# Kernel optimization log

Hardware: AMD Instinct MI355X
Metric: run time of the kernel (lower is better)

Reference implementation:

```python
import jax, jax.numpy as jnp
import numpy as np

BETA = 0.95
THR = 1.0
NUM_STEPS = 100
ALPHA = 2.0  # snntorch atan surrogate default

@jax.custom_vjp
def atan_spike(x):
    return (x > 0).astype(x.dtype)

def _as_fwd(x):
    return (x > 0).astype(x.dtype), x

def _as_bwd(x, g):
    return (g * (ALPHA / 2) / (1 + (jnp.pi / 2 * ALPHA * x) ** 2),)

atan_spike.defvjp(_as_fwd, _as_bwd)


def setup_inputs() -> dict:
    key = jax.random.key(0)
    ks = jax.random.split(key, 9)
    B = 16384
    SH, NH, CO, OUT = 1024, 1024, 256, 64
    s = 0.05
    return {
        "x": jax.random.normal(ks[0], (B, 105), jnp.float32),
        "snn_w1": jax.random.normal(ks[1], (SH, 5), jnp.float32) * s,
        "snn_b1": jnp.zeros((SH,), jnp.float32),
        "snn_w2": jax.random.normal(ks[2], (OUT, SH), jnp.float32) * s,
        "snn_b2": jnp.zeros((OUT,), jnp.float32),
        "nn_w1": jax.random.normal(ks[3], (NH, 5), jnp.float32) * s,
        "nn_b1": jnp.zeros((NH,), jnp.float32),
        "nn_w2": jax.random.normal(ks[4], (OUT, NH), jnp.float32) * s,
        "nn_b2": jnp.zeros((OUT,), jnp.float32),
        "conv_w": jax.random.normal(ks[5], (32, 1, 3), jnp.float32) * s,
        "conv_b": jnp.zeros((32,), jnp.float32),
        "cnn_fc_w": jax.random.normal(ks[6], (CO, 32 * 50), jnp.float32) * s,
        "cnn_fc_b": jnp.zeros((CO,), jnp.float32),
        "comb_w": jax.random.normal(ks[7], (OUT, 2 * OUT + CO), jnp.float32) * s,
        "comb_b": jnp.zeros((OUT,), jnp.float32),
    }


def _forward(x, snn_w1, snn_b1, snn_w2, snn_b2, nn_w1, nn_b1, nn_w2, nn_b2,
             conv_w, conv_b, cnn_fc_w, cnn_fc_b, comb_w, comb_b):
    feats = x[:, :5]                 # [B,5]
    wave = x[:, 5:][:, None, :]      # [B,1,100]
    B = x.shape[0]

    # ---- SNN branch (LIF, beta leak, subtract reset, threshold 1.0) ----
    cur1 = feats @ snn_w1.T + snn_b1  # input current is constant across steps

    def step(carry, _):
        mem1, spk1, mem2, spk2 = carry
        # reset term uses detached spike (snntorch mem_reset detaches)
        mem1 = BETA * mem1 + cur1 - jax.lax.stop_gradient(spk1) * THR
        spk1 = atan_spike(mem1 - THR)
        cur2 = spk1 @ snn_w2.T + snn_b2
        mem2 = BETA * mem2 + cur2 - jax.lax.stop_gradient(spk2) * THR
        spk2 = atan_spike(mem2 - THR)
        return (mem1, spk1, mem2, spk2), spk2

    z1 = jnp.zeros_like(cur1)
    z2 = jnp.zeros((B, snn_w2.shape[0]), cur1.dtype)
    _, spk_rec = jax.lax.scan(step, (z1, z1, z2, z2), None, length=NUM_STEPS)
    snn_out = spk_rec.mean(axis=0)   # [B,OUT]

    # ---- MLP branch ----
    nn_out = jax.nn.relu(feats @ nn_w1.T + nn_b1) @ nn_w2.T + nn_b2

    # ---- CNN branch ----
    c = jax.lax.conv_general_dilated(wave, conv_w, (1,), [(1, 1)],
                                     dimension_numbers=("NCW", "OIW", "NCW"))
    c = jax.nn.relu(c + conv_b[None, :, None])   # [B,32,100]
    c = c.reshape(B, 32, 50, 2).max(axis=-1)      # MaxPool1d(k=2,s=2)
    cnn_out = c.reshape(B, -1) @ cnn_fc_w.T + cnn_fc_b

    combined = jnp.concatenate([snn_out, nn_out, cnn_out], axis=1)
    return combined @ comb_w.T + comb_b


def reference(x, snn_w1, snn_b1, snn_w2, snn_b2, nn_w1, nn_b1, nn_w2, nn_b2,
              conv_w, conv_b, cnn_fc_w, cnn_fc_b, comb_w, comb_b):
    return _forward(x, snn_w1, snn_b1, snn_w2, snn_b2, nn_w1, nn_b1, nn_w2,
                    nn_b2, conv_w, conv_b, cnn_fc_w, cnn_fc_b, comb_w, comb_b)
```

## Files before the change

kernel.cpp:

```cpp
#include <hip/hip_runtime.h>

typedef __bf16 bf16x8_t __attribute__((ext_vector_type(8)));
typedef float f32x4_t __attribute__((ext_vector_type(4)));

#define NSTEPS 100
#define COMBF 51200u

static __device__ __forceinline__ unsigned short f2bfu(float v) {
  union { __bf16 h; unsigned short u; } c; c.h = (__bf16)v; return c.u;
}
static __device__ __forceinline__ unsigned int pack2bf(float a, float b) {
  return (unsigned)f2bfu(a) | ((unsigned)f2bfu(b) << 16);
}
union BF8U { unsigned int u[4]; bf16x8_t v; };

static __device__ __forceinline__ bf16x8_t bfrag_f32(const float* __restrict__ p, float s) {
  BF8U r;
#pragma unroll
  for (int i = 0; i < 4; ++i) r.u[i] = pack2bf(p[2*i]*s, p[2*i+1]*s);
  return r.v;
}

static __device__ __forceinline__ void comb_store(unsigned char* ldsp, int k, int row, float v) {
  *(unsigned short*)(ldsp + COMBF +
      (unsigned)((k >> 5)*1024 + (((k >> 3) & 3)*16 + row)*16 + (k & 7)*2)) = f2bfu(v);
}

__global__ __launch_bounds__(512, 2)
void hybrid_v3(const float* __restrict__ x,
               const float* __restrict__ snn_w1, const float* __restrict__ snn_b1,
               const float* __restrict__ snn_w2, const float* __restrict__ snn_b2,
               const float* __restrict__ nn_w1,  const float* __restrict__ nn_b1,
               const float* __restrict__ nn_w2,  const float* __restrict__ nn_b2,
               const float* __restrict__ conv_w, const float* __restrict__ conv_b,
               const float* __restrict__ fc_w,   const float* __restrict__ fc_b,
               const float* __restrict__ comb_w, const float* __restrict__ comb_b,
               const unsigned short* __restrict__ fcwb, int use_bf,
               float* __restrict__ out)
{
  __shared__ __align__(16) unsigned char lds[65536];
  const int tid  = threadIdx.x;
  const int w    = tid >> 6;
  const int l    = tid & 63;
  const int q    = l >> 4;
  const int m    = l & 15;
  const int row0 = blockIdx.x * 16;

  const int hi  = w >> 2;
  const int ntr = w & 3;
  const int rn  = ntr*16 + m;
  const int rA  = hi*4 + q;
  const int rB  = rA + 8;

  const float* xr = x + (row0 + m)*105;
  const float f0 = xr[0], f1 = xr[1], f2 = xr[2], f3 = xr[3], f4 = xr[4];
  const float b2l = snn_b2[rn];

  bf16x8_t bfr[4][4];
#pragma unroll
  for (int ci = 0; ci < 4; ++ci)
#pragma unroll
    for (int nt = 0; nt < 4; ++nt)
      bfr[ci][nt] = bfrag_f32(snn_w2 + (nt*16 + m)*1024 + (w*4 + ci)*32 + q*8, 1.f);

  float c[32], mem[32];
  {
    const int kb = w*128 + q*8;
#pragma unroll
    for (int ci = 0; ci < 4; ++ci) {
      const float* wp = snn_w1 + (kb + ci*32)*5;
      float wa[40];
#pragma unroll
      for (int u2 = 0; u2 < 10; ++u2) {
        const float4 t4 = *(const float4*)(wp + u2*4);
        wa[u2*4+0] = t4.x; wa[u2*4+1] = t4.y; wa[u2*4+2] = t4.z; wa[u2*4+3] = t4.w;
      }
#pragma unroll
      for (int j = 0; j < 8; ++j) {
        c[ci*8+j] = f0*wa[j*5] + f1*wa[j*5+1] + f2*wa[j*5+2] + f3*wa[j*5+3] + f4*wa[j*5+4]
                  + snn_b1[kb + ci*32 + j];
        mem[ci*8+j] = 0.f;
      }
    }
  }

  BF8U afr[4];
  auto lif_update_pack = [&]() {
#pragma unroll
    for (int i = 0; i < 32; ++i) {
      const float sp = mem[i] > 1.f ? 1.f : 0.f;
      mem[i] = __fsub_rn(__fadd_rn(__fmul_rn(0.95f, mem[i]), c[i]), sp);
    }
#pragma unroll
    for (int ci = 0; ci < 4; ++ci)
#pragma unroll
      for (int jj = 0; jj < 4; ++jj)
        afr[ci].u[jj] = (mem[ci*8 + 2*jj]   > 1.f ? 0x3F80u     : 0u)
                      | (mem[ci*8 + 2*jj+1] > 1.f ? 0x3F800000u : 0u);
  };
  lif_update_pack();

  float m2A = 0.f, s2A = 0.f, cntA = 0.f;
  float m2B = 0.f, s2B = 0.f, cntB = 0.f;

  const unsigned pbase = (unsigned)(ntr*1024 + hi*256 + m*16 + q*4);
  const f32x4_t z4 = {0.f, 0.f, 0.f, 0.f};

#pragma unroll 1
  for (int t = 0; t < NSTEPS; ++t) {
    f32x4_t acc[4] = {z4, z4, z4, z4};
#pragma unroll
    for (int ci = 0; ci < 4; ++ci) {
#pragma unroll
      for (int nt = 0; nt < 4; ++nt)
        acc[nt] = __builtin_amdgcn_mfma_f32_16x16x32_bf16(afr[ci].v, bfr[ci][nt], acc[nt], 0,0,0);
    }
#pragma unroll
    for (int nt = 0; nt < 4; ++nt)
      *(f32x4_t*)(lds + (unsigned)(((w*4 + nt)*64 + l)*16)) = acc[nt];
    __syncthreads();
    float vA[8], vB[8];
#pragma unroll
    for (int s = 0; s < 8; ++s) vA[s] = *(const float*)(lds + pbase + (unsigned)(s*4096));
#pragma unroll
    for (int s = 0; s < 8; ++s) vB[s] = *(const float*)(lds + pbase + 512u + (unsigned)(s*4096));
    if (t < NSTEPS - 1) lif_update_pack();
    {
      float curA = (((vA[0]+vA[1]) + (vA[2]+vA[3])) + ((vA[4]+vA[5]) + (vA[6]+vA[7]))) + b2l;
      float curB = (((vB[0]+vB[1]) + (vB[2]+vB[3])) + ((vB[4]+vB[5]) + (vB[6]+vB[7]))) + b2l;
      m2A = __fsub_rn(__fadd_rn(__fmul_rn(0.95f, m2A), curA), s2A);
      s2A = m2A > 1.f ? 1.f : 0.f;  cntA += s2A;
      m2B = __fsub_rn(__fadd_rn(__fmul_rn(0.95f, m2B), curB), s2B);
      s2B = m2B > 1.f ? 1.f : 0.f;  cntB += s2B;
    }
    __syncthreads();
  }

#pragma unroll
  for (int ci = 0; ci < 4; ++ci)
#pragma unroll
    for (int nt = 0; nt < 4; ++nt)
      bfr[ci][nt] = bfrag_f32(nn_w2 + (nt*16 + m)*1024 + (w*4 + ci)*32 + q*8, 1.f);
  {
    BF8U hfr[4];
    const int kb = w*128 + q*8;
#pragma unroll
    for (int ci = 0; ci < 4; ++ci) {
      const float* wp = nn_w1 + (kb + ci*32)*5;
      float wa[40];
#pragma unroll
      for (int u2 = 0; u2 < 10; ++u2) {
        const float4 t4 = *(const float4*)(wp + u2*4);
        wa[u2*4+0] = t4.x; wa[u2*4+1] = t4.y; wa[u2*4+2] = t4.z; wa[u2*4+3] = t4.w;
      }
      float hv[8];
#pragma unroll
      for (int j = 0; j < 8; ++j) {
        const float h = f0*wa[j*5] + f1*wa[j*5+1] + f2*wa[j*5+2] + f3*wa[j*5+3] + f4*wa[j*5+4]
                      + nn_b1[kb + ci*32 + j];
        hv[j] = fmaxf(h, 0.f);
      }
#pragma unroll
      for (int jj = 0; jj < 4; ++jj) hfr[ci].u[jj] = pack2bf(hv[2*jj], hv[2*jj+1]);
    }
    f32x4_t acc[4] = {z4, z4, z4, z4};
#pragma unroll
    for (int ci = 0; ci < 4; ++ci)
#pragma unroll
      for (int nt = 0; nt < 4; ++nt)
        acc[nt] = __builtin_amdgcn_mfma_f32_16x16x32_bf16(hfr[ci].v, bfr[ci][nt], acc[nt], 0,0,0);
#pragma unroll
    for (int nt = 0; nt < 4; ++nt)
      *(f32x4_t*)(lds + (unsigned)(((w*4 + nt)*64 + l)*16)) = acc[nt];
  }
  __syncthreads();
  {
    float vA[8], vB[8];
#pragma unroll
    for (int s = 0; s < 8; ++s) vA[s] = *(const float*)(lds + pbase + (unsigned)(s*4096));
#pragma unroll
    for (int s = 0; s < 8; ++s) vB[s] = *(const float*)(lds + pbase + 512u + (unsigned)(s*4096));
    const float nA = (((vA[0]+vA[1]) + (vA[2]+vA[3])) + ((vA[4]+vA[5]) + (vA[6]+vA[7]))) + nn_b2[rn];
    const float nB = (((vB[0]+vB[1]) + (vB[2]+vB[3])) + ((vB[4]+vB[5]) + (vB[6]+vB[7]))) + nn_b2[rn];
    comb_store(lds, rn,      rA, cntA * 0.0078125f);
    comb_store(lds, rn,      rB, cntB * 0.0078125f);
    comb_store(lds, 64 + rn, rA, nA);
    comb_store(lds, 64 + rn, rB, nB);
  }
  __syncthreads();

  {
    const int ch = tid >> 4;
    const float cw0 = conv_w[ch*3+0], cw1 = conv_w[ch*3+1], cw2 = conv_w[ch*3+2];
    const float cbb = conv_b[ch];
    const float* xw = xr + 5;
    float xm1 = 0.f, x0v = xw[0];
#pragma unroll 1
    for (int p = 0; p < 50; ++p) {
      const float xp1 = xw[2*p + 1];
      const float xp2 = (p < 49) ? xw[2*p + 2] : 0.f;
      const float av = cw0*xm1 + cw1*x0v + cw2*xp1 + cbb;
      const float bv = cw0*x0v + cw1*xp1 + cw2*xp2 + cbb;
      const float pv = fmaxf(fmaxf(av, 0.f), fmaxf(bv, 0.f));
      const int k = ch*50 + p;
      *(unsigned short*)(lds + (unsigned)((k>>5)*1024 + (((k>>3)&3)*16 + m)*16 + (k&7)*2)) = f2bfu(pv);
      xm1 = xp1; x0v = xp2;
    }
  }
  __syncthreads();

  {
    const int c0 = (w*2 + 0)*16 + m;
    const int c1 = (w*2 + 1)*16 + m;
    f32x4_t e0 = z4, o0 = z4, e1 = z4, o1 = z4;
    if (use_bf) {
#pragma unroll 2
      for (int kc = 0; kc < 50; kc += 2) {
        const bf16x8_t a0 = *(const bf16x8_t*)(lds + (unsigned)((kc*64 + l)*16));
        const bf16x8_t a1 = *(const bf16x8_t*)(lds + (unsigned)(((kc+1)*64 + l)*16));
        e0 = __builtin_amdgcn_mfma_f32_16x16x32_bf16(a0, *(const bf16x8_t*)(fcwb + c0*1600 + kc*32 + q*8), e0, 0,0,0);
        o0 = __builtin_amdgcn_mfma_f32_16x16x32_bf16(a1, *(const bf16x8_t*)(fcwb + c0*1600 + (kc+1)*32 + q*8), o0, 0,0,0);
        e1 = __builtin_amdgcn_mfma_f32_16x16x32_bf16(a0, *(const bf16x8_t*)(fcwb + c1*1600 + kc*32 + q*8), e1, 0,0,0);
        o1 = __builtin_amdgcn_mfma_f32_16x16x32_bf16(a1, *(const bf16x8_t*)(fcwb + c1*1600 + (kc+1)*32 + q*8), o1, 0,0,0);
      }
    } else {
#pragma unroll 2
      for (int kc = 0; kc < 50; kc += 2) {
        const bf16x8_t a0 = *(const bf16x8_t*)(lds + (unsigned)((kc*64 + l)*16));
        const bf16x8_t a1 = *(const bf16x8_t*)(lds + (unsigned)(((kc+1)*64 + l)*16));
        e0 = __builtin_amdgcn_mfma_f32_16x16x32_bf16(a0, bfrag_f32(fc_w + c0*1600 + kc*32 + q*8, 1.f), e0, 0,0,0);
        o0 = __builtin_amdgcn_mfma_f32_16x16x32_bf16(a1, bfrag_f32(fc_w + c0*1600 + (kc+1)*32 + q*8, 1.f), o0, 0,0,0);
        e1 = __builtin_amdgcn_mfma_f32_16x16x32_bf16(a0, bfrag_f32(fc_w + c1*1600 + kc*32 + q*8, 1.f), e1, 0,0,0);
        o1 = __builtin_amdgcn_mfma_f32_16x16x32_bf16(a1, bfrag_f32(fc_w + c1*1600 + (kc+1)*32 + q*8, 1.f), o1, 0,0,0);
      }
    }
    const float fb0 = fc_b[c0], fb1 = fc_b[c1];
#pragma unroll
    for (int r = 0; r < 4; ++r) {
      comb_store(lds, 128 + c0, q*4 + r, (e0[r] + o0[r]) + fb0);
      comb_store(lds, 128 + c1, q*4 + r, (e1[r] + o1[r]) + fb1);
    }
  }
  __syncthreads();

  if (w < 4) {
    const int cn = w*16 + m;
    f32x4_t oe = z4, oo = z4;
#pragma unroll
    for (int kc = 0; kc < 12; kc += 2) {
      const bf16x8_t a0 = *(const bf16x8_t*)(lds + COMBF + (unsigned)((kc*64 + l)*16));
      const bf16x8_t a1 = *(const bf16x8_t*)(lds + COMBF + (unsigned)(((kc+1)*64 + l)*16));
      const float s0 = (kc    < 2) ? 1.28f : 1.f;
      const float s1 = (kc+1 < 2) ? 1.28f : 1.f;
      oe = __builtin_amdgcn_mfma_f32_16x16x32_bf16(a0, bfrag_f32(comb_w + cn*384 + kc*32 + q*8, s0), oe, 0,0,0);
      oo = __builtin_amdgcn_mfma_f32_16x16x32_bf16(a1, bfrag_f32(comb_w + cn*384 + (kc+1)*32 + q*8, s1), oo, 0,0,0);
    }
    const float cb2 = comb_b[cn];
#pragma unroll
    for (int r = 0; r < 4; ++r)
      out[(row0 + q*4 + r)*64 + cn] = (oe[r] + oo[r]) + cb2;
  }
}

__global__ __launch_bounds__(256)
void fcw_to_bf16(const float* __restrict__ src, unsigned short* __restrict__ dst) {
  const int i = (blockIdx.x * 256 + threadIdx.x) * 4;
  const float4 v = *(const float4*)(src + i);
  ushort4 o;
  o.x = f2bfu(v.x); o.y = f2bfu(v.y); o.z = f2bfu(v.z); o.w = f2bfu(v.w);
  *(ushort4*)(dst + i) = o;
}

extern "C" void kernel_launch(void* const* d_in, const int* in_sizes, int n_in,
                              void* d_out, int out_size, void* d_ws, size_t ws_size,
                              hipStream_t stream) {
  const float* x       = (const float*)d_in[0];
  const float* snn_w1  = (const float*)d_in[1];
  const float* snn_b1  = (const float*)d_in[2];
  const float* snn_w2  = (const float*)d_in[3];
  const float* snn_b2  = (const float*)d_in[4];
  const float* nn_w1   = (const float*)d_in[5];
  const float* nn_b1   = (const float*)d_in[6];
  const float* nn_w2   = (const float*)d_in[7];
  const float* nn_b2   = (const float*)d_in[8];
  const float* conv_w  = (const float*)d_in[9];
  const float* conv_b  = (const float*)d_in[10];
  const float* fc_w    = (const float*)d_in[11];
  const float* fc_b    = (const float*)d_in[12];
  const float* comb_w  = (const float*)d_in[13];
  const float* comb_b  = (const float*)d_in[14];
  float* outp = (float*)d_out;

  const int rows = in_sizes[0] / 105;
  const int grid = rows / 16;

  const size_t fcw_elems = (size_t)in_sizes[11];
  const int use_bf = (ws_size >= fcw_elems * 2) ? 1 : 0;
  unsigned short* fcwb = (unsigned short*)d_ws;
  if (use_bf) {
    fcw_to_bf16<<<dim3((unsigned)(fcw_elems / 1024)), dim3(256), 0, stream>>>(fc_w, fcwb);
  }

  hybrid_v3<<<dim3(grid), dim3(512), 0, stream>>>(
      x, snn_w1, snn_b1, snn_w2, snn_b2,
      nn_w1, nn_b1, nn_w2, nn_b2,
      conv_w, conv_b, fc_w, fc_b, comb_w, comb_b,
      fcwb, use_bf, outp);
}
```

Before: 840.7 us.

## Double-buffer SNN partial-sum exchange to halve barriers per timestep

The 100-step LIF loop now ping-pongs between two LDS buffers for the cross-wave partial sums. Each phase reads the previous step's partials while issuing the current step's MFMAs and writes, so one __syncthreads per step is enough instead of two. The second-layer membrane update lags by one step, with a final drain after the loop. This removes a barrier per step and lets LDS reads overlap MFMA work, at the cost of using 64 KB of LDS space for the two buffers plus the combined region and slightly more complex sequencing.

```diff
diff --git a/kernel.cpp b/kernel.cpp
--- a/kernel.cpp
+++ b/kernel.cpp
@@ -4,6 +4,8 @@
 typedef float f32x4_t __attribute__((ext_vector_type(4)));
 
 #define NSTEPS 100
+#define PB0 0u
+#define PB1 32768u
 #define COMBF 51200u
 
 static __device__ __forceinline__ unsigned short f2bfu(float v) {
@@ -27,7 +29,7 @@
 }
 
 __global__ __launch_bounds__(512, 2)
-void hybrid_v3(const float* __restrict__ x,
+void hybrid_v4(const float* __restrict__ x,
                const float* __restrict__ snn_w1, const float* __restrict__ snn_b1,
                const float* __restrict__ snn_w2, const float* __restrict__ snn_b2,
                const float* __restrict__ nn_w1,  const float* __restrict__ nn_b1,
@@ -103,29 +105,29 @@
   float m2A = 0.f, s2A = 0.f, cntA = 0.f;
   float m2B = 0.f, s2B = 0.f, cntB = 0.f;
 
-  const unsigned pbase = (unsigned)(ntr*1024 + hi*256 + m*16 + q*4);
+  const unsigned pbase  = (unsigned)(ntr*1024 + hi*256 + m*16 + q*4);
+  const unsigned wtbase = (unsigned)((w*4*64 + l)*16);
   const f32x4_t z4 = {0.f, 0.f, 0.f, 0.f};
 
-#pragma unroll 1
-  for (int t = 0; t < NSTEPS; ++t) {
+  auto phase = [&](unsigned cur, unsigned prv, bool doRead, bool doLif) {
+    float vA[8], vB[8];
+    if (doRead) {
+#pragma unroll
+      for (int s = 0; s < 8; ++s) vA[s] = *(const float*)(lds + prv + pbase + (unsigned)(s*4096));
+#pragma unroll
+      for (int s = 0; s < 8; ++s) vB[s] = *(const float*)(lds + prv + pbase + 512u + (unsigned)(s*4096));
+    }
     f32x4_t acc[4] = {z4, z4, z4, z4};
 #pragma unroll
-    for (int ci = 0; ci < 4; ++ci) {
+    for (int ci = 0; ci < 4; ++ci)
 #pragma unroll
       for (int nt = 0; nt < 4; ++nt)
         acc[nt] = __builtin_amdgcn_mfma_f32_16x16x32_bf16(afr[ci].v, bfr[ci][nt], acc[nt], 0,0,0);
-    }
 #pragma unroll
     for (int nt = 0; nt < 4; ++nt)
-      *(f32x4_t*)(lds + (unsigned)(((w*4 + nt)*64 + l)*16)) = acc[nt];
-    __syncthreads();
-    float vA[8], vB[8];
-#pragma unroll
-    for (int s = 0; s < 8; ++s) vA[s] = *(const float*)(lds + pbase + (unsigned)(s*4096));
-#pragma unroll
-    for (int s = 0; s < 8; ++s) vB[s] = *(const float*)(lds + pbase + 512u + (unsigned)(s*4096));
-    if (t < NSTEPS - 1) lif_update_pack();
-    {
+      *(f32x4_t*)(lds + cur + wtbase + (unsigned)(nt*1024)) = acc[nt];
+    if (doLif) lif_update_pack();
+    if (doRead) {
       float curA = (((vA[0]+vA[1]) + (vA[2]+vA[3])) + ((vA[4]+vA[5]) + (vA[6]+vA[7]))) + b2l;
       float curB = (((vB[0]+vB[1]) + (vB[2]+vB[3])) + ((vB[4]+vB[5]) + (vB[6]+vB[7]))) + b2l;
       m2A = __fsub_rn(__fadd_rn(__fmul_rn(0.95f, m2A), curA), s2A);
@@ -134,6 +136,12 @@
       s2B = m2B > 1.f ? 1.f : 0.f;  cntB += s2B;
     }
     __syncthreads();
+  };
+
+#pragma unroll 1
+  for (int tt = 0; tt < NSTEPS; tt += 2) {
+    phase(PB0, PB1, tt > 0, true);
+    phase(PB1, PB0, true,  tt + 1 < NSTEPS - 1);
   }
 
 #pragma unroll
@@ -142,6 +150,18 @@
     for (int nt = 0; nt < 4; ++nt)
       bfr[ci][nt] = bfrag_f32(nn_w2 + (nt*16 + m)*1024 + (w*4 + ci)*32 + q*8, 1.f);
   {
+    float vA[8], vB[8];
+#pragma unroll
+    for (int s = 0; s < 8; ++s) vA[s] = *(const float*)(lds + PB1 + pbase + (unsigned)(s*4096));
+#pragma unroll
+    for (int s = 0; s < 8; ++s) vB[s] = *(const float*)(lds + PB1 + pbase + 512u + (unsigned)(s*4096));
+    float curA = (((vA[0]+vA[1]) + (vA[2]+vA[3])) + ((vA[4]+vA[5]) + (vA[6]+vA[7]))) + b2l;
+    float curB = (((vB[0]+vB[1]) + (vB[2]+vB[3])) + ((vB[4]+vB[5]) + (vB[6]+vB[7]))) + b2l;
+    m2A = __fsub_rn(__fadd_rn(__fmul_rn(0.95f, m2A), curA), s2A);
+    s2A = m2A > 1.f ? 1.f : 0.f;  cntA += s2A;
+    m2B = __fsub_rn(__fadd_rn(__fmul_rn(0.95f, m2B), curB), s2B);
+    s2B = m2B > 1.f ? 1.f : 0.f;  cntB += s2B;
+
     BF8U hfr[4];
     const int kb = w*128 + q*8;
 #pragma unroll
@@ -171,15 +191,15 @@
         acc[nt] = __builtin_amdgcn_mfma_f32_16x16x32_bf16(hfr[ci].v, bfr[ci][nt], acc[nt], 0,0,0);
 #pragma unroll
     for (int nt = 0; nt < 4; ++nt)
-      *(f32x4_t*)(lds + (unsigned)(((w*4 + nt)*64 + l)*16)) = acc[nt];
+      *(f32x4_t*)(lds + PB0 + wtbase + (unsigned)(nt*1024)) = acc[nt];
   }
   __syncthreads();
   {
     float vA[8], vB[8];
 #pragma unroll
-    for (int s = 0; s < 8; ++s) vA[s] = *(const float*)(lds + pbase + (unsigned)(s*4096));
-#pragma unroll
-    for (int s = 0; s < 8; ++s) vB[s] = *(const float*)(lds + pbase + 512u + (unsigned)(s*4096));
+    for (int s = 0; s < 8; ++s) vA[s] = *(const float*)(lds + PB0 + pbase + (unsigned)(s*4096));
+#pragma unroll
+    for (int s = 0; s < 8; ++s) vB[s] = *(const float*)(lds + PB0 + pbase + 512u + (unsigned)(s*4096));
     const float nA = (((vA[0]+vA[1]) + (vA[2]+vA[3])) + ((vA[4]+vA[5]) + (vA[6]+vA[7]))) + nn_b2[rn];
     const float nB = (((vB[0]+vB[1]) + (vB[2]+vB[3])) + ((vB[4]+vB[5]) + (vB[6]+vB[7]))) + nn_b2[rn];
     comb_store(lds, rn,      rA, cntA * 0.0078125f);
@@ -301,7 +321,7 @@
     fcw_to_bf16<<<dim3((unsigned)(fcw_elems / 1024)), dim3(256), 0, stream>>>(fc_w, fcwb);
   }
 
-  hybrid_v3<<<dim3(grid), dim3(512), 0, stream>>>(
+  hybrid_v4<<<dim3(grid), dim3(512), 0, stream>>>(
       x, snn_w1, snn_b1, snn_w2, snn_b2,
       nn_w1, nn_b1, nn_w2, nn_b2,
       conv_w, conv_b, fc_w, fc_b, comb_w, comb_b,
```

Result: faster. 722.1 us (-14.1%).

## Replace per-step block barriers with 4-deep LDS ring and atomic counters

Applied to the files above, without the earlier changes.

Each SNN timestep's partial MFMA results now go to one of four LDS buffers. Waves signal completion through workgroup-scope atomic counters instead of two __syncthreads per step. A wave can compute step t's MFMA while step t-1's reduction is consumed, which removes the full-block barrier stalls. The cost is 128KB+ of dynamic LDS per block, which drops occupancy to one block per CU despite the launch bound, plus spin-wait polling overhead.

```diff
diff --git a/kernel.cpp b/kernel.cpp
--- a/kernel.cpp
+++ b/kernel.cpp
@@ -4,7 +4,7 @@
 typedef float f32x4_t __attribute__((ext_vector_type(4)));
 
 #define NSTEPS 100
-#define COMBF 51200u
+#define COMBF 118784u
 
 static __device__ __forceinline__ unsigned short f2bfu(float v) {
   union { __bf16 h; unsigned short u; } c; c.h = (__bf16)v; return c.u;
@@ -27,7 +27,7 @@
 }
 
 __global__ __launch_bounds__(512, 2)
-void hybrid_v3(const float* __restrict__ x,
+void hybrid_v7(const float* __restrict__ x,
                const float* __restrict__ snn_w1, const float* __restrict__ snn_b1,
                const float* __restrict__ snn_w2, const float* __restrict__ snn_b2,
                const float* __restrict__ nn_w1,  const float* __restrict__ nn_b1,
@@ -38,8 +38,11 @@
                const unsigned short* __restrict__ fcwb, int use_bf,
                float* __restrict__ out)
 {
-  __shared__ __align__(16) unsigned char lds[65536];
+  extern __shared__ __align__(16) unsigned char lds[];
+  __shared__ unsigned wcnt[4];
   const int tid  = threadIdx.x;
+  if (tid < 4) wcnt[tid] = 0u;
+
   const int w    = tid >> 6;
   const int l    = tid & 63;
   const int q    = l >> 4;
@@ -103,38 +106,66 @@
   float m2A = 0.f, s2A = 0.f, cntA = 0.f;
   float m2B = 0.f, s2B = 0.f, cntB = 0.f;
 
-  const unsigned pbase = (unsigned)(ntr*1024 + hi*256 + m*16 + q*4);
+  const unsigned pbase  = (unsigned)(ntr*1024 + hi*256 + m*16 + q*4);
+  const unsigned wtbase = (unsigned)((w*4*64 + l)*16);
   const f32x4_t z4 = {0.f, 0.f, 0.f, 0.f};
+
+  __syncthreads();
 
 #pragma unroll 1
   for (int t = 0; t < NSTEPS; ++t) {
+    const unsigned cur = (unsigned)(t & 3) * 32768u;
     f32x4_t acc[4] = {z4, z4, z4, z4};
 #pragma unroll
-    for (int ci = 0; ci < 4; ++ci) {
+    for (int ci = 0; ci < 4; ++ci)
 #pragma unroll
       for (int nt = 0; nt < 4; ++nt)
         acc[nt] = __builtin_amdgcn_mfma_f32_16x16x32_bf16(afr[ci].v, bfr[ci][nt], acc[nt], 0,0,0);
-    }
 #pragma unroll
     for (int nt = 0; nt < 4; ++nt)
-      *(f32x4_t*)(lds + (unsigned)(((w*4 + nt)*64 + l)*16)) = acc[nt];
-    __syncthreads();
-    float vA[8], vB[8];
-#pragma unroll
-    for (int s = 0; s < 8; ++s) vA[s] = *(const float*)(lds + pbase + (unsigned)(s*4096));
-#pragma unroll
-    for (int s = 0; s < 8; ++s) vB[s] = *(const float*)(lds + pbase + 512u + (unsigned)(s*4096));
-    if (t < NSTEPS - 1) lif_update_pack();
-    {
+      *(f32x4_t*)(lds + cur + wtbase + (unsigned)(nt*1024)) = acc[nt];
+    if (l == 0)
+      __hip_atomic_fetch_add(&wcnt[t & 3], 1u, __ATOMIC_RELEASE, __HIP_MEMORY_SCOPE_WORKGROUP);
+    if (t > 0) {
+      const int tp = t - 1;
+      const unsigned pb = (unsigned)(tp & 3) * 32768u;
+      const unsigned target = 8u * ((unsigned)(tp >> 2) + 1u);
+      while (__hip_atomic_load(&wcnt[tp & 3], __ATOMIC_ACQUIRE, __HIP_MEMORY_SCOPE_WORKGROUP) < target)
+        __builtin_amdgcn_s_sleep(2);
+      float vA[8], vB[8];
+#pragma unroll
+      for (int s = 0; s < 8; ++s) vA[s] = *(const float*)(lds + pb + pbase + (unsigned)(s*4096));
+#pragma unroll
+      for (int s = 0; s < 8; ++s) vB[s] = *(const float*)(lds + pb + pbase + 512u + (unsigned)(s*4096));
+      if (t < NSTEPS - 1) lif_update_pack();
       float curA = (((vA[0]+vA[1]) + (vA[2]+vA[3])) + ((vA[4]+vA[5]) + (vA[6]+vA[7]))) + b2l;
       float curB = (((vB[0]+vB[1]) + (vB[2]+vB[3])) + ((vB[4]+vB[5]) + (vB[6]+vB[7]))) + b2l;
       m2A = __fsub_rn(__fadd_rn(__fmul_rn(0.95f, m2A), curA), s2A);
       s2A = m2A > 1.f ? 1.f : 0.f;  cntA += s2A;
       m2B = __fsub_rn(__fadd_rn(__fmul_rn(0.95f, m2B), curB), s2B);
       s2B = m2B > 1.f ? 1.f : 0.f;  cntB += s2B;
-    }
-    __syncthreads();
-  }
+    } else {
+      lif_update_pack();
+    }
+  }
+  {
+    const unsigned target = 8u * ((unsigned)(99 >> 2) + 1u);
+    while (__hip_atomic_load(&wcnt[3], __ATOMIC_ACQUIRE, __HIP_MEMORY_SCOPE_WORKGROUP) < target)
+      __builtin_amdgcn_s_sleep(2);
+    const unsigned pb = 3u * 32768u;
+    float vA[8], vB[8];
+#pragma unroll
+    for (int s = 0; s < 8; ++s) vA[s] = *(const float*)(lds + pb + pbase + (unsigned)(s*4096));
+#pragma unroll
+    for (int s = 0; s < 8; ++s) vB[s] = *(const float*)(lds + pb + pbase + 512u + (unsigned)(s*4096));
+    float curA = (((vA[0]+vA[1]) + (vA[2]+vA[3])) + ((vA[4]+vA[5]) + (vA[6]+vA[7]))) + b2l;
+    float curB = (((vB[0]+vB[1]) + (vB[2]+vB[3])) + ((vB[4]+vB[5]) + (vB[6]+vB[7]))) + b2l;
+    m2A = __fsub_rn(__fadd_rn(__fmul_rn(0.95f, m2A), curA), s2A);
+    s2A = m2A > 1.f ? 1.f : 0.f;  cntA += s2A;
+    m2B = __fsub_rn(__fadd_rn(__fmul_rn(0.95f, m2B), curB), s2B);
+    s2B = m2B > 1.f ? 1.f : 0.f;  cntB += s2B;
+  }
+  __syncthreads();
 
 #pragma unroll
   for (int ci = 0; ci < 4; ++ci)
@@ -171,7 +202,7 @@
         acc[nt] = __builtin_amdgcn_mfma_f32_16x16x32_bf16(hfr[ci].v, bfr[ci][nt], acc[nt], 0,0,0);
 #pragma unroll
     for (int nt = 0; nt < 4; ++nt)
-      *(f32x4_t*)(lds + (unsigned)(((w*4 + nt)*64 + l)*16)) = acc[nt];
+      *(f32x4_t*)(lds + wtbase + (unsigned)(nt*1024)) = acc[nt];
   }
   __syncthreads();
   {
@@ -294,6 +325,9 @@
   const int rows = in_sizes[0] / 105;
   const int grid = rows / 16;
 
+  (void)hipFuncSetAttribute((const void*)hybrid_v7,
+                            hipFuncAttributeMaxDynamicSharedMemorySize, 131072);
+
   const size_t fcw_elems = (size_t)in_sizes[11];
   const int use_bf = (ws_size >= fcw_elems * 2) ? 1 : 0;
   unsigned short* fcwb = (unsigned short*)d_ws;
@@ -301,7 +335,7 @@
     fcw_to_bf16<<<dim3((unsigned)(fcw_elems / 1024)), dim3(256), 0, stream>>>(fc_w, fcwb);
   }
 
-  hybrid_v3<<<dim3(grid), dim3(512), 0, stream>>>(
+  hybrid_v7<<<dim3(grid), dim3(512), 131072, stream>>>(
       x, snn_w1, snn_b1, snn_w2, snn_b2,
       nn_w1, nn_b1, nn_w2, nn_b2,
       conv_w, conv_b, fc_w, fc_b, comb_w, comb_b,
```

New measurement: 878.7 us. 1.05x slower.
